# Performance work log

Measured on AMD Instinct MI355X. Metric: run time of the kernel, lower is better.

The kernel has to match this reference:

```python
import jax, jax.numpy as jnp
import numpy as np

NUM_HEADS = 16
D_K = 8  # == n_qubits


def setup_inputs() -> dict:
    key = jax.random.key(0)
    k1, k2, k3 = jax.random.split(key, 3)
    x = jax.random.normal(k1, (4, 2048, 128), dtype=jnp.float32)
    # trainable RX angles, one per qubit (tq.RX has_params=True)
    theta = jax.random.normal(k2, (D_K,), dtype=jnp.float32)
    # out_proj: Linear(embed_dim, embed_dim, bias=False)
    w_out = jax.random.normal(k3, (128, 128), dtype=jnp.float32) * (1.0 / np.sqrt(128.0))
    return {"x": x, "theta": theta, "w_out": w_out}


def quantum_features(x, theta):
    # x: [b, s, e]. Per head of size d_k: encode RX(x_i), trainable RX(theta_i)
    # (composes to RX(x_i + theta_i)), CNOT ladder [i, i+1], measure PauliZ.
    # Heisenberg picture: Z_w -> Z_0...Z_w, so <Z_w> = prod_{i<=w} cos(x_i + theta_i).
    b, s, e = x.shape
    heads = x.reshape(b, s, NUM_HEADS, D_K)
    return jnp.cumprod(jnp.cos(heads + theta), axis=-1)  # [b, s, h, d_k]


def reference(x, theta, w_out):
    b, s, e = x.shape
    # q == k == v: same shared q_layer applied to the same x three times.
    qkv = quantum_features(x, theta)            # [b, s, h, d_k]
    q = qkv.transpose(0, 2, 1, 3)               # [b, h, s, d_k]
    scores = jnp.einsum('bhqd,bhkd->bhqk', q, q) / np.sqrt(D_K)
    attn = jax.nn.softmax(scores, axis=-1)      # dropout is identity at eval
    out = jnp.einsum('bhqk,bhkd->bhqd', attn, q)
    out = out.transpose(0, 2, 1, 3).reshape(b, s, e)
    return out @ w_out.T
```

## Files before the change

### kernel.cpp

```cpp
#include <hip/hip_runtime.h>

#define BATCH 4
#define SEQ   2048
#define EMB   128
#define NH    16
#define DK    8

#define QSCALE 0.510069726f

typedef _Float16 v2h __attribute__((ext_vector_type(2)));
typedef _Float16 v4h __attribute__((ext_vector_type(4)));
typedef __fp16   v2fp __attribute__((ext_vector_type(2)));
typedef float    v4f __attribute__((ext_vector_type(4)));

#define CHUNK  512
#define NCHUNK (SEQ / CHUNK)
#define VTP    520

__launch_bounds__(256, 6)
__global__ void attn_kernel(const float* __restrict__ x,
                            const float* __restrict__ theta,
                            _Float16* __restrict__ Ah ) {
  __shared__ __align__(16) _Float16 Kl[CHUNK * 8];
  __shared__ __align__(16) _Float16 VT[16][VTP];

  const int tid  = threadIdx.x;
  const int L    = tid & 63;
  const int quad = L >> 4;
  const int ln   = L & 15;
  const int wv   = tid >> 6;
  const int bh     = blockIdx.x >> 4;
  const int qchunk = blockIdx.x & 15;
  const int qb     = qchunk * 128 + wv * 32;
  const int b = bh >> 4;
  const int h = bh & 15;

  float th[DK];
#pragma unroll
  for (int i = 0; i < DK; ++i) th[i] = theta[i];

  for (int i = tid; i < 8 * VTP / 4; i += 256) {
    v4h v = (i < VTP / 4) ? (v4h){(_Float16)1.f, (_Float16)1.f,
                                  (_Float16)1.f, (_Float16)1.f}
                          : (v4h){0, 0, 0, 0};
    *(v4h*)(&VT[8][0] + i * 4) = v;
  }

  const int c0 = qchunk >> 2;
  v4h qf[2] = {{0, 0, 0, 0}, {0, 0, 0, 0}};
  v4f acc[2];
  acc[0] = (v4f){0.f, 0.f, 0.f, 0.f};
  acc[1] = (v4f){0.f, 0.f, 0.f, 0.f};
  const v4f zf = (v4f){0.f, 0.f, 0.f, 0.f};

  for (int cc = 0; cc < NCHUNK; ++cc) {
    const int c = (c0 + cc) & (NCHUNK - 1);
    if (cc) __syncthreads();

    {
      const int k2 = tid * 2;
      const float* xp = x + ((size_t)b * SEQ + c * CHUNK + k2) * EMB + h * DK;
      const float4 a0 = *(const float4*)(xp);
      const float4 a1 = *(const float4*)(xp + 4);
      const float4 b0 = *(const float4*)(xp + EMB);
      const float4 b1 = *(const float4*)(xp + EMB + 4);

      float r0[8], r1[8];
      r0[0] = __cosf(a0.x + th[0]);
      r0[1] = r0[0] * __cosf(a0.y + th[1]);
      r0[2] = r0[1] * __cosf(a0.z + th[2]);
      r0[3] = r0[2] * __cosf(a0.w + th[3]);
      r0[4] = r0[3] * __cosf(a1.x + th[4]);
      r0[5] = r0[4] * __cosf(a1.y + th[5]);
      r0[6] = r0[5] * __cosf(a1.z + th[6]);
      r0[7] = r0[6] * __cosf(a1.w + th[7]);
      r1[0] = __cosf(b0.x + th[0]);
      r1[1] = r1[0] * __cosf(b0.y + th[1]);
      r1[2] = r1[1] * __cosf(b0.z + th[2]);
      r1[3] = r1[2] * __cosf(b0.w + th[3]);
      r1[4] = r1[3] * __cosf(b1.x + th[4]);
      r1[5] = r1[4] * __cosf(b1.y + th[5]);
      r1[6] = r1[5] * __cosf(b1.z + th[6]);
      r1[7] = r1[6] * __cosf(b1.w + th[7]);

      _Float16 h0[8], h1[8];
#pragma unroll
      for (int i = 0; i < 8; ++i) { h0[i] = (_Float16)r0[i]; h1[i] = (_Float16)r1[i]; }

      union { v4h v[2]; float4 f; } u0, u1;
      u0.v[0] = (v4h){h0[0], h0[1], h0[2], h0[3]};
      u0.v[1] = (v4h){h0[4], h0[5], h0[6], h0[7]};
      u1.v[0] = (v4h){h1[0], h1[1], h1[2], h1[3]};
      u1.v[1] = (v4h){h1[4], h1[5], h1[6], h1[7]};
      *(float4*)&Kl[k2 * 8]     = u0.f;
      *(float4*)&Kl[k2 * 8 + 8] = u1.f;

#pragma unroll
      for (int d = 0; d < 8; ++d) {
        v2h w = {h0[d], h1[d]};
        *(v2h*)&VT[d][k2] = w;
      }
    }
    __syncthreads();

    if (cc == 0) {
      const v4h qsc = {(_Float16)QSCALE, (_Float16)QSCALE,
                       (_Float16)QSCALE, (_Float16)QSCALE};
      const int lbase = qb - c0 * CHUNK + ln;
      if (quad < 2) {
        qf[0] = *(const v4h*)&Kl[(lbase)      * 8 + quad * 4] * qsc;
        qf[1] = *(const v4h*)&Kl[(lbase + 16) * 8 + quad * 4] * qsc;
      }
    }

#pragma unroll 4
    for (int t16 = 0; t16 < CHUNK / 16; ++t16) {
      const v4h kf = *(const v4h*)&Kl[(t16 * 16 + ln) * 8 + (quad & 1) * 4];
      const v4h vt = *(const v4h*)&VT[ln][t16 * 16 + quad * 4];
#pragma unroll
      for (int t = 0; t < 2; ++t) {
        const v4f s = __builtin_amdgcn_mfma_f32_16x16x16f16(kf, qf[t], zf, 0, 0, 0);
        union { v2fp p[2]; v4h v; } pk;
        pk.p[0] = __builtin_amdgcn_cvt_pkrtz(__builtin_amdgcn_exp2f(s[0]),
                                             __builtin_amdgcn_exp2f(s[1]));
        pk.p[1] = __builtin_amdgcn_cvt_pkrtz(__builtin_amdgcn_exp2f(s[2]),
                                             __builtin_amdgcn_exp2f(s[3]));
        acc[t] = __builtin_amdgcn_mfma_f32_16x16x16f16(vt, pk.v, acc[t], 0, 0, 0);
      }
    }
  }

#pragma unroll
  for (int t = 0; t < 2; ++t) {
    const float den = __shfl(acc[t][0], 32 + ln, 64);
    const float inv = 1.0f / den;
    if (quad < 2) {
      const int qrow = qb + t * 16 + ln;
      v4h o = {(_Float16)(acc[t][0] * inv), (_Float16)(acc[t][1] * inv),
               (_Float16)(acc[t][2] * inv), (_Float16)(acc[t][3] * inv)};
      *(v4h*)(Ah + ((size_t)b * SEQ + qrow) * EMB + h * DK + quad * 4) = o;
    }
  }
}

__launch_bounds__(256, 4)
__global__ void proj_kernel(const _Float16* __restrict__ Ah,
                            const float* __restrict__ W,
                            float* __restrict__ out) {
  __shared__ __align__(16) _Float16 Ahs[64][136];
  __shared__ __align__(16) _Float16 Whs[64][136];

  const int tid  = threadIdx.x;
  const int L    = tid & 63;
  const int wv   = tid >> 6;
  const int quad = L >> 4;
  const int ln   = L & 15;
  const int rowbase = blockIdx.x * 64;
  const int colbase = blockIdx.y * 64;

#pragma unroll
  for (int it = 0; it < 4; ++it) {
    const int idx = it * 256 + tid;
    const int r  = idx >> 4;
    const int c8 = idx & 15;
    *(uint4*)&Ahs[r][c8 * 8] =
        *(const uint4*)(Ah + (size_t)(rowbase + r) * EMB + c8 * 8);
  }
#pragma unroll
  for (int it = 0; it < 8; ++it) {
    const int idx = it * 256 + tid;
    const int n  = idx >> 5;
    const int c4 = idx & 31;
    const float4 w = *(const float4*)(W + (size_t)(colbase + n) * EMB + c4 * 4);
    v4h wh = {(_Float16)w.x, (_Float16)w.y, (_Float16)w.z, (_Float16)w.w};
    *(v4h*)&Whs[n][c4 * 4] = wh;
  }
  __syncthreads();

  v4f acc[4];
#pragma unroll
  for (int nt = 0; nt < 4; ++nt) acc[nt] = (v4f){0.f, 0.f, 0.f, 0.f};

#pragma unroll
  for (int k8 = 0; k8 < 8; ++k8) {
    const v4h af = *(const v4h*)&Ahs[wv * 16 + ln][k8 * 16 + quad * 4];
#pragma unroll
    for (int nt = 0; nt < 4; ++nt) {
      const v4h bf = *(const v4h*)&Whs[nt * 16 + ln][k8 * 16 + quad * 4];
      acc[nt] = __builtin_amdgcn_mfma_f32_16x16x16f16(af, bf, acc[nt], 0, 0, 0);
    }
  }

#pragma unroll
  for (int nt = 0; nt < 4; ++nt) {
    const int col = colbase + nt * 16 + ln;
#pragma unroll
    for (int r = 0; r < 4; ++r) {
      out[(size_t)(rowbase + wv * 16 + quad * 4 + r) * EMB + col] = acc[nt][r];
    }
  }
}

extern "C" void kernel_launch(void* const* d_in, const int* in_sizes, int n_in,
                              void* d_out, int out_size, void* d_ws, size_t ws_size,
                              hipStream_t stream) {
  const float* x     = (const float*)d_in[0];
  const float* theta = (const float*)d_in[1];
  const float* w_out = (const float*)d_in[2];
  float* out = (float*)d_out;

  _Float16* Ah = (_Float16*)d_ws;

  attn_kernel<<<dim3(1024), dim3(256), 0, stream>>>(x, theta, Ah);

  proj_kernel<<<dim3((BATCH * SEQ) / 64, 2), dim3(256), 0, stream>>>(Ah, w_out, out);
}
```

Measured before the change: 94.16 us.

## Prefetch next chunk's x into registers during attention compute

Loads the x values for the next key chunk into registers right after the LDS barrier, so global-memory latency overlaps with the MFMA/exp loop of the current chunk. It also changes the row assignment from two adjacent rows per thread to rows tid and tid+256, so VT stores become single-half writes instead of packed pairs. The cost is extra live registers (16 floats) under the occupancy-6 launch bound, and more, narrower LDS stores for the transposed V.

```diff
diff --git a/kernel.cpp b/kernel.cpp
--- a/kernel.cpp
+++ b/kernel.cpp
@@ -47,6 +47,17 @@
   }
 
   const int c0 = qchunk >> 2;
+  const float* xb = x + (size_t)b * SEQ * EMB + h * DK;
+
+  float4 pa0, pa1, pb0, pb1;
+  {
+    const float* xp = xb + (size_t)(c0 * CHUNK + tid) * EMB;
+    pa0 = *(const float4*)(xp);
+    pa1 = *(const float4*)(xp + 4);
+    pb0 = *(const float4*)(xp + 256 * EMB);
+    pb1 = *(const float4*)(xp + 256 * EMB + 4);
+  }
+
   v4h qf[2] = {{0, 0, 0, 0}, {0, 0, 0, 0}};
   v4f acc[2];
   acc[0] = (v4f){0.f, 0.f, 0.f, 0.f};
@@ -54,34 +65,26 @@
   const v4f zf = (v4f){0.f, 0.f, 0.f, 0.f};
 
   for (int cc = 0; cc < NCHUNK; ++cc) {
-    const int c = (c0 + cc) & (NCHUNK - 1);
     if (cc) __syncthreads();
 
     {
-      const int k2 = tid * 2;
-      const float* xp = x + ((size_t)b * SEQ + c * CHUNK + k2) * EMB + h * DK;
-      const float4 a0 = *(const float4*)(xp);
-      const float4 a1 = *(const float4*)(xp + 4);
-      const float4 b0 = *(const float4*)(xp + EMB);
-      const float4 b1 = *(const float4*)(xp + EMB + 4);
-
       float r0[8], r1[8];
-      r0[0] = __cosf(a0.x + th[0]);
-      r0[1] = r0[0] * __cosf(a0.y + th[1]);
-      r0[2] = r0[1] * __cosf(a0.z + th[2]);
-      r0[3] = r0[2] * __cosf(a0.w + th[3]);
-      r0[4] = r0[3] * __cosf(a1.x + th[4]);
-      r0[5] = r0[4] * __cosf(a1.y + th[5]);
-      r0[6] = r0[5] * __cosf(a1.z + th[6]);
-      r0[7] = r0[6] * __cosf(a1.w + th[7]);
-      r1[0] = __cosf(b0.x + th[0]);
-      r1[1] = r1[0] * __cosf(b0.y + th[1]);
-      r1[2] = r1[1] * __cosf(b0.z + th[2]);
-      r1[3] = r1[2] * __cosf(b0.w + th[3]);
-      r1[4] = r1[3] * __cosf(b1.x + th[4]);
-      r1[5] = r1[4] * __cosf(b1.y + th[5]);
-      r1[6] = r1[5] * __cosf(b1.z + th[6]);
-      r1[7] = r1[6] * __cosf(b1.w + th[7]);
+      r0[0] = __cosf(pa0.x + th[0]);
+      r0[1] = r0[0] * __cosf(pa0.y + th[1]);
+      r0[2] = r0[1] * __cosf(pa0.z + th[2]);
+      r0[3] = r0[2] * __cosf(pa0.w + th[3]);
+      r0[4] = r0[3] * __cosf(pa1.x + th[4]);
+      r0[5] = r0[4] * __cosf(pa1.y + th[5]);
+      r0[6] = r0[5] * __cosf(pa1.z + th[6]);
+      r0[7] = r0[6] * __cosf(pa1.w + th[7]);
+      r1[0] = __cosf(pb0.x + th[0]);
+      r1[1] = r1[0] * __cosf(pb0.y + th[1]);
+      r1[2] = r1[1] * __cosf(pb0.z + th[2]);
+      r1[3] = r1[2] * __cosf(pb0.w + th[3]);
+      r1[4] = r1[3] * __cosf(pb1.x + th[4]);
+      r1[5] = r1[4] * __cosf(pb1.y + th[5]);
+      r1[6] = r1[5] * __cosf(pb1.z + th[6]);
+      r1[7] = r1[6] * __cosf(pb1.w + th[7]);
 
       _Float16 h0[8], h1[8];
 #pragma unroll
@@ -92,16 +95,25 @@
       u0.v[1] = (v4h){h0[4], h0[5], h0[6], h0[7]};
       u1.v[0] = (v4h){h1[0], h1[1], h1[2], h1[3]};
       u1.v[1] = (v4h){h1[4], h1[5], h1[6], h1[7]};
-      *(float4*)&Kl[k2 * 8]     = u0.f;
-      *(float4*)&Kl[k2 * 8 + 8] = u1.f;
+      *(float4*)&Kl[tid * 8]         = u0.f;
+      *(float4*)&Kl[(tid + 256) * 8] = u1.f;
 
 #pragma unroll
       for (int d = 0; d < 8; ++d) {
-        v2h w = {h0[d], h1[d]};
-        *(v2h*)&VT[d][k2] = w;
+        VT[d][tid]       = h0[d];
+        VT[d][tid + 256] = h1[d];
       }
     }
     __syncthreads();
+
+    if (cc + 1 < NCHUNK) {
+      const int cn = (c0 + cc + 1) & (NCHUNK - 1);
+      const float* xp = xb + (size_t)(cn * CHUNK + tid) * EMB;
+      pa0 = *(const float4*)(xp);
+      pa1 = *(const float4*)(xp + 4);
+      pb0 = *(const float4*)(xp + 256 * EMB);
+      pb1 = *(const float4*)(xp + 256 * EMB + 4);
+    }
 
     if (cc == 0) {
       const v4h qsc = {(_Float16)QSCALE, (_Float16)QSCALE,
```

Result: no change. 95.95 us (+1.9%).

## Double-buffer K/V chunks in LDS with register prefetch of next chunk

Applied to the files above, without the earlier changes.

Halves the key chunk to 256 rows and double-buffers the K and V-transpose LDS tiles, so the global load of the next chunk is issued into registers while the current chunk runs its MFMA work. Staging of the next buffer (cos/cumprod plus LDS writes) is interleaved before the compute loop, leaving one barrier per chunk. This is meant to hide global memory latency behind the exp/MFMA loop. In exchange it takes a few more registers, runs twice as many chunk iterations, and drops the unroll pragma on the inner loop.

```diff
diff --git a/kernel.cpp b/kernel.cpp
--- a/kernel.cpp
+++ b/kernel.cpp
@@ -13,16 +13,16 @@
 typedef __fp16   v2fp __attribute__((ext_vector_type(2)));
 typedef float    v4f __attribute__((ext_vector_type(4)));
 
-#define CHUNK  512
+#define CHUNK  256
 #define NCHUNK (SEQ / CHUNK)
-#define VTP    520
+#define VTPAD  264
 
 __launch_bounds__(256, 6)
 __global__ void attn_kernel(const float* __restrict__ x,
                             const float* __restrict__ theta,
                             _Float16* __restrict__ Ah ) {
-  __shared__ __align__(16) _Float16 Kl[CHUNK * 8];
-  __shared__ __align__(16) _Float16 VT[16][VTP];
+  __shared__ __align__(16) _Float16 Kl[2][CHUNK * 8];
+  __shared__ __align__(16) _Float16 VT[2][16][VTPAD];
 
   const int tid  = threadIdx.x;
   const int L    = tid & 63;
@@ -39,84 +39,80 @@
 #pragma unroll
   for (int i = 0; i < DK; ++i) th[i] = theta[i];
 
-  for (int i = tid; i < 8 * VTP / 4; i += 256) {
-    v4h v = (i < VTP / 4) ? (v4h){(_Float16)1.f, (_Float16)1.f,
-                                  (_Float16)1.f, (_Float16)1.f}
-                          : (v4h){0, 0, 0, 0};
-    *(v4h*)(&VT[8][0] + i * 4) = v;
-  }
-
-  const int c0 = qchunk >> 2;
+#pragma unroll
+  for (int bfi = 0; bfi < 2; ++bfi) {
+    for (int i = tid; i < 8 * VTPAD / 4; i += 256) {
+      v4h v = (i < VTPAD / 4) ? (v4h){(_Float16)1.f, (_Float16)1.f,
+                                      (_Float16)1.f, (_Float16)1.f}
+                              : (v4h){0, 0, 0, 0};
+      *(v4h*)(&VT[bfi][8][0] + i * 4) = v;
+    }
+  }
+
+  const int c0 = qchunk >> 1;
+  const float* xb = x + (size_t)b * SEQ * EMB + h * DK;
+
+  float4 pa0, pa1;
+
+#define PREFETCH(cidx)                                                     \
+  {                                                                        \
+    const float* xp = xb + (size_t)((cidx) * CHUNK + tid) * EMB;           \
+    pa0 = *(const float4*)(xp);                                            \
+    pa1 = *(const float4*)(xp + 4);                                        \
+  }
+
+#define STAGE(bfi)                                                         \
+  {                                                                        \
+    float r[8];                                                            \
+    r[0] = __cosf(pa0.x + th[0]);                                          \
+    r[1] = r[0] * __cosf(pa0.y + th[1]);                                   \
+    r[2] = r[1] * __cosf(pa0.z + th[2]);                                   \
+    r[3] = r[2] * __cosf(pa0.w + th[3]);                                   \
+    r[4] = r[3] * __cosf(pa1.x + th[4]);                                   \
+    r[5] = r[4] * __cosf(pa1.y + th[5]);                                   \
+    r[6] = r[5] * __cosf(pa1.z + th[6]);                                   \
+    r[7] = r[6] * __cosf(pa1.w + th[7]);                                   \
+    _Float16 hv[8];                                                        \
+    for (int i = 0; i < 8; ++i) hv[i] = (_Float16)r[i];                    \
+    union { v4h v[2]; float4 f; } u;                                       \
+    u.v[0] = (v4h){hv[0], hv[1], hv[2], hv[3]};                            \
+    u.v[1] = (v4h){hv[4], hv[5], hv[6], hv[7]};                            \
+    *(float4*)&Kl[bfi][tid * 8] = u.f;       \
+    for (int d = 0; d < 8; ++d) VT[bfi][d][tid] = hv[d];                   \
+  }
+
+  PREFETCH(c0);
+  STAGE(0);
+  PREFETCH((c0 + 1) & (NCHUNK - 1));
+  __syncthreads();
+
   v4h qf[2] = {{0, 0, 0, 0}, {0, 0, 0, 0}};
+  {
+    const v4h qsc = {(_Float16)QSCALE, (_Float16)QSCALE,
+                     (_Float16)QSCALE, (_Float16)QSCALE};
+    const int lbase = (qchunk & 1) * 128 + wv * 32 + ln;
+    if (quad < 2) {
+      qf[0] = *(const v4h*)&Kl[0][(lbase)      * 8 + quad * 4] * qsc;
+      qf[1] = *(const v4h*)&Kl[0][(lbase + 16) * 8 + quad * 4] * qsc;
+    }
+  }
+
   v4f acc[2];
   acc[0] = (v4f){0.f, 0.f, 0.f, 0.f};
   acc[1] = (v4f){0.f, 0.f, 0.f, 0.f};
   const v4f zf = (v4f){0.f, 0.f, 0.f, 0.f};
 
   for (int cc = 0; cc < NCHUNK; ++cc) {
-    const int c = (c0 + cc) & (NCHUNK - 1);
-    if (cc) __syncthreads();
-
-    {
-      const int k2 = tid * 2;
-      const float* xp = x + ((size_t)b * SEQ + c * CHUNK + k2) * EMB + h * DK;
-      const float4 a0 = *(const float4*)(xp);
-      const float4 a1 = *(const float4*)(xp + 4);
-      const float4 b0 = *(const float4*)(xp + EMB);
-      const float4 b1 = *(const float4*)(xp + EMB + 4);
-
-      float r0[8], r1[8];
-      r0[0] = __cosf(a0.x + th[0]);
-      r0[1] = r0[0] * __cosf(a0.y + th[1]);
-      r0[2] = r0[1] * __cosf(a0.z + th[2]);
-      r0[3] = r0[2] * __cosf(a0.w + th[3]);
-      r0[4] = r0[3] * __cosf(a1.x + th[4]);
-      r0[5] = r0[4] * __cosf(a1.y + th[5]);
-      r0[6] = r0[5] * __cosf(a1.z + th[6]);
-      r0[7] = r0[6] * __cosf(a1.w + th[7]);
-      r1[0] = __cosf(b0.x + th[0]);
-      r1[1] = r1[0] * __cosf(b0.y + th[1]);
-      r1[2] = r1[1] * __cosf(b0.z + th[2]);
-      r1[3] = r1[2] * __cosf(b0.w + th[3]);
-      r1[4] = r1[3] * __cosf(b1.x + th[4]);
-      r1[5] = r1[4] * __cosf(b1.y + th[5]);
-      r1[6] = r1[5] * __cosf(b1.z + th[6]);
-      r1[7] = r1[6] * __cosf(b1.w + th[7]);
-
-      _Float16 h0[8], h1[8];
-#pragma unroll
-      for (int i = 0; i < 8; ++i) { h0[i] = (_Float16)r0[i]; h1[i] = (_Float16)r1[i]; }
-
-      union { v4h v[2]; float4 f; } u0, u1;
-      u0.v[0] = (v4h){h0[0], h0[1], h0[2], h0[3]};
-      u0.v[1] = (v4h){h0[4], h0[5], h0[6], h0[7]};
-      u1.v[0] = (v4h){h1[0], h1[1], h1[2], h1[3]};
-      u1.v[1] = (v4h){h1[4], h1[5], h1[6], h1[7]};
-      *(float4*)&Kl[k2 * 8]     = u0.f;
-      *(float4*)&Kl[k2 * 8 + 8] = u1.f;
-
-#pragma unroll
-      for (int d = 0; d < 8; ++d) {
-        v2h w = {h0[d], h1[d]};
-        *(v2h*)&VT[d][k2] = w;
-      }
-    }
-    __syncthreads();
-
-    if (cc == 0) {
-      const v4h qsc = {(_Float16)QSCALE, (_Float16)QSCALE,
-                       (_Float16)QSCALE, (_Float16)QSCALE};
-      const int lbase = qb - c0 * CHUNK + ln;
-      if (quad < 2) {
-        qf[0] = *(const v4h*)&Kl[(lbase)      * 8 + quad * 4] * qsc;
-        qf[1] = *(const v4h*)&Kl[(lbase + 16) * 8 + quad * 4] * qsc;
-      }
-    }
-
-#pragma unroll 4
+    const int cur = cc & 1;
+
+    if (cc + 1 < NCHUNK) {
+      STAGE(1 - cur);
+      if (cc + 2 < NCHUNK) PREFETCH((c0 + cc + 2) & (NCHUNK - 1));
+    }
+
     for (int t16 = 0; t16 < CHUNK / 16; ++t16) {
-      const v4h kf = *(const v4h*)&Kl[(t16 * 16 + ln) * 8 + (quad & 1) * 4];
-      const v4h vt = *(const v4h*)&VT[ln][t16 * 16 + quad * 4];
+      const v4h kf = *(const v4h*)&Kl[cur][(t16 * 16 + ln) * 8 + (quad & 1) * 4];
+      const v4h vt = *(const v4h*)&VT[cur][ln][t16 * 16 + quad * 4];
 #pragma unroll
       for (int t = 0; t < 2; ++t) {
         const v4f s = __builtin_amdgcn_mfma_f32_16x16x16f16(kf, qf[t], zf, 0, 0, 0);
@@ -128,6 +124,7 @@
         acc[t] = __builtin_amdgcn_mfma_f32_16x16x16f16(vt, pk.v, acc[t], 0, 0, 0);
       }
     }
+    __syncthreads();
   }
 
 #pragma unroll
@@ -141,6 +138,8 @@
       *(v4h*)(Ah + ((size_t)b * SEQ + qrow) * EMB + h * DK + quad * 4) = o;
     }
   }
+#undef PREFETCH
+#undef STAGE
 }
 
 __launch_bounds__(256, 4)
```

After: 96.10 us. 2.1% more time.
